# Optimization experiments

Hardware: AMD Instinct MI355X
Metric: run time of the kernel (lower is better)

The kernel has to match this reference:

```python
import jax, jax.numpy as jnp
import numpy as np

D_MODEL = 2048
N_HEADS = 16
HEAD_DIM = D_MODEL // N_HEADS  # 128
B, S, PAST = 2, 2048, 2048


def setup_inputs() -> dict:
    key = jax.random.key(0)
    ks = jax.random.split(key, 7)
    sc = 0.02
    return {
        "x": jax.random.normal(ks[0], (B, S, D_MODEL), dtype=jnp.float32),
        "past_k": jax.random.normal(ks[1], (B, N_HEADS, PAST, HEAD_DIM), dtype=jnp.float32),
        "past_v": jax.random.normal(ks[2], (B, N_HEADS, PAST, HEAD_DIM), dtype=jnp.float32),
        "Wq": jax.random.normal(ks[3], (D_MODEL, D_MODEL), dtype=jnp.float32) * sc,
        "Wk": jax.random.normal(ks[4], (D_MODEL, D_MODEL), dtype=jnp.float32) * sc,
        "Wv": jax.random.normal(ks[5], (D_MODEL, D_MODEL), dtype=jnp.float32) * sc,
        "Wo": jax.random.normal(ks[6], (D_MODEL, D_MODEL), dtype=jnp.float32) * sc,
    }


def reference(x, past_k, past_v, Wq, Wk, Wv, Wo):
    b, s, d = x.shape
    # nn.Linear(bias=False): y = x @ W.T ; split heads -> (B, H, S, hd)
    def proj_heads(W):
        return (x @ W.T).reshape(b, s, N_HEADS, HEAD_DIM).transpose(0, 2, 1, 3)
    q = proj_heads(Wq)
    k = proj_heads(Wk)
    v = proj_heads(Wv)
    # KV-cache append along sequence axis
    k = jnp.concatenate([past_k, k], axis=2)  # (B, H, full_S, hd)
    v = jnp.concatenate([past_v, v], axis=2)
    present = (k, v)
    full_s = k.shape[2]
    scores = jnp.einsum("bhqd,bhkd->bhqk", q, k) / (HEAD_DIM ** 0.5)
    # causal mask: query i (global pos past+i) may attend keys j <= past+i
    offset = full_s - s
    qi = jnp.arange(s)[:, None]
    kj = jnp.arange(full_s)[None, :]
    mask = kj > (qi + offset)  # triu with diagonal = full_s - s + 1
    scores = jnp.where(mask[None, None], -jnp.inf, scores)
    attn = jax.nn.softmax(scores, axis=-1)
    out = jnp.einsum("bhqk,bhkd->bhqd", attn, v)
    out = out.transpose(0, 2, 1, 3).reshape(b, s, d)
    output = out @ Wo.T
    return output, present
```

## Files before the change

### kernel.cpp

```cpp
#include <hip/hip_runtime.h>
#include <hip/hip_bf16.h>
#include <stdint.h>

typedef __attribute__((ext_vector_type(8))) short bf16x8;
typedef __attribute__((ext_vector_type(4))) float f32x4;
typedef __attribute__((ext_vector_type(16))) float f32x16;
typedef unsigned short u16;
typedef unsigned int u32;
typedef const __attribute__((address_space(1))) u32* gp_t;
typedef __attribute__((address_space(3))) u32* lp_t;

#define HD 128
#define NH 16
#define SEQ 2048
#define PASTN 2048
#define FULLS 4096
#define DM 2048

__device__ __forceinline__ u16 f2b(float f){
  union { float f; u32 u; } v; v.f = f;
  return (u16)((v.u + 0x7fffu + ((v.u >> 16) & 1u)) >> 16);
}
__device__ __forceinline__ float b2f(u16 b){
  union { u32 u; float f; } v; v.u = ((u32)b) << 16;
  return v.f;
}
__device__ __forceinline__ u32 cvtpk(float lo, float hi){
  u32 r; asm("v_cvt_pk_bf16_f32 %0, %1, %2" : "=v"(r) : "v"(lo), "v"(hi)); return r;
}
__device__ __forceinline__ f32x16 zero16(){ f32x16 z = {}; return z; }

__global__ void k_conv5(const float* __restrict__ sx,
                        const float* __restrict__ s1, const float* __restrict__ s2,
                        const float* __restrict__ s3, const float* __restrict__ s4,
                        u16* __restrict__ dx,
                        u16* __restrict__ d1, u16* __restrict__ d2,
                        u16* __restrict__ d3, u16* __restrict__ d4)
{
  const int total = 2097152 + 4 * 1048576;
  int i = blockIdx.x * blockDim.x + threadIdx.x;
  int stride = gridDim.x * blockDim.x;
  for (; i < total; i += stride){
    const float* s; u16* d; int off;
    if (i < 2097152){ s = sx; d = dx; off = i; }
    else {
      int t = i - 2097152;
      int seg = t >> 20; off = t & 1048575;
      s = (seg == 0) ? s1 : (seg == 1) ? s2 : (seg == 2) ? s3 : s4;
      d = (seg == 0) ? d1 : (seg == 1) ? d2 : (seg == 2) ? d3 : d4;
    }
    float4 v = ((const float4*)s)[off];
    ushort4 o = { f2b(v.x), f2b(v.y), f2b(v.z), f2b(v.w) };
    ((ushort4*)d)[off] = o;
  }
}

__global__ void k_past_k(const float* __restrict__ pk, float* __restrict__ outk,
                         u16* __restrict__ kb, int n4){
  int i = blockIdx.x * blockDim.x + threadIdx.x;
  int stride = gridDim.x * blockDim.x;
  for (; i < n4; i += stride){
    int g = i * 4;
    int c = g & 127;
    int r = g >> 7;
    int bh = r >> 11;
    int s = r & 2047;
    long dst = ((long)bh * FULLS + s) * HD + c;
    float4 v = ((const float4*)pk)[i];
    *(float4*)(outk + dst) = v;
    ushort4 o = { f2b(v.x), f2b(v.y), f2b(v.z), f2b(v.w) };
    *(ushort4*)(kb + dst) = o;
  }
}

__global__ void k_past_v(const float* __restrict__ pv, float* __restrict__ outv,
                         u16* __restrict__ vtb){
  __shared__ float tile[32][33];
  int bh = blockIdx.z;
  int d0 = blockIdx.x * 32;
  int s0 = blockIdx.y * 32;
  int tx = threadIdx.x, ty = threadIdx.y;
  const float* src = pv + (long)bh * PASTN * HD;
  float* dstv = outv + (long)bh * FULLS * HD;
#pragma unroll
  for (int k = 0; k < 4; k++){
    int si = ty + 8 * k;
    float v = src[(long)(s0 + si) * HD + d0 + tx];
    dstv[(long)(s0 + si) * HD + d0 + tx] = v;
    tile[si][tx] = v;
  }
  __syncthreads();
  u16* dstt = vtb + (long)bh * HD * FULLS;
#pragma unroll
  for (int k = 0; k < 4; k++){
    int di = ty + 8 * k;
    dstt[(long)(d0 + di) * FULLS + (s0 + tx)] = f2b(tile[tx][di]);
  }
}

__global__ void k_gemm_qkv(const u16* __restrict__ A,
                           const u16* __restrict__ Bq, const u16* __restrict__ Bk,
                           const u16* __restrict__ Bv,
                           u16* __restrict__ qb, u16* __restrict__ kbb,
                           u16* __restrict__ vtb,
                           float* __restrict__ outk, float* __restrict__ outv)
{
  __shared__ u16 As[128 * 64];
  __shared__ u16 Bs[128 * 64];
  const int K = DM;
  const int tid = threadIdx.x;
  const int w = tid >> 6, l = tid & 63;
  const int m0 = blockIdx.y * 128, n0 = blockIdx.x * 128;
  const int which = n0 >> 11;
  const u16* Bm = (which == 0) ? Bq : (which == 1) ? Bk : Bv;
  const int nbase = n0 & 2047;
  const int wr = w >> 1, wc = w & 1;
  const int lr = l & 15;
  const int lkb = (l >> 4) * 16;
  f32x4 acc[4][4] = {};

  for (int kt = 0; kt < K; kt += 64){
#pragma unroll
    for (int it = 0; it < 4; it++){
      int Pw = it * 4096 + w * 1024;
      int P = Pw + l * 16;
      int row = P >> 7, cb = P & 127;
      const u16* ga = A + (long)(m0 + row) * K + kt + (cb >> 1);
      __builtin_amdgcn_global_load_lds((gp_t)(const void*)ga, (lp_t)(void*)((char*)As + Pw), 16, 0, 0);
      const u16* gb = Bm + (long)(nbase + row) * K + kt + (cb >> 1);
      __builtin_amdgcn_global_load_lds((gp_t)(const void*)gb, (lp_t)(void*)((char*)Bs + Pw), 16, 0, 0);
    }
    __syncthreads();
#pragma unroll
    for (int kk = 0; kk < 2; kk++){
      bf16x8 af[4], bf[4];
#pragma unroll
      for (int i = 0; i < 4; i++){
        af[i] = *(const bf16x8*)((const char*)As + (wr * 64 + i * 16 + lr) * 128 + kk * 64 + lkb);
        bf[i] = *(const bf16x8*)((const char*)Bs + (wc * 64 + i * 16 + lr) * 128 + kk * 64 + lkb);
      }
#pragma unroll
      for (int i = 0; i < 4; i++)
#pragma unroll
        for (int j = 0; j < 4; j++)
          acc[i][j] = __builtin_amdgcn_mfma_f32_16x16x32_bf16(af[i], bf[j], acc[i][j], 0, 0, 0);
    }
    __syncthreads();
  }

  const int rbase = m0 + wr * 64 + ((l >> 4) << 2);
  const int cbase = wc * 64 + lr;
#pragma unroll
  for (int i = 0; i < 4; i++){
#pragma unroll
    for (int j = 0; j < 4; j++){
      const int nl = (nbase + cbase + j * 16);
      const int h = nl >> 7, dd = nl & 127;
      if (which == 2){
        const int mm = rbase + i * 16;
        const int b = mm >> 11, s = mm & 2047;
        const int bh = b * NH + h;
        ushort4 pk = { f2b(acc[i][j][0]), f2b(acc[i][j][1]), f2b(acc[i][j][2]), f2b(acc[i][j][3]) };
        *(ushort4*)(vtb + ((long)bh * HD + dd) * FULLS + PASTN + s) = pk;
#pragma unroll
        for (int r = 0; r < 4; r++){
          long idx = ((long)bh * FULLS + PASTN + s + r) * HD + dd;
          outv[idx] = acc[i][j][r];
        }
      } else if (which == 1){
#pragma unroll
        for (int r = 0; r < 4; r++){
          const int mm = rbase + i * 16 + r;
          const int b = mm >> 11, s = mm & 2047;
          long idx = (((long)(b * NH + h)) * FULLS + PASTN + s) * HD + dd;
          float v = acc[i][j][r];
          kbb[idx] = f2b(v);
          outk[idx] = v;
        }
      } else {
#pragma unroll
        for (int r = 0; r < 4; r++){
          const int mm = rbase + i * 16 + r;
          const int b = mm >> 11, s = mm & 2047;
          qb[(((long)(b * NH + h)) * SEQ + s) * HD + dd] = f2b(acc[i][j][r]);
        }
      }
    }
  }
}

__global__ void k_gemm_o(const u16* __restrict__ A, const u16* __restrict__ Bm,
                         float* __restrict__ outf, int M, int N, int K)
{
  __shared__ u16 As[128 * 64];
  __shared__ u16 Bs[128 * 64];
  const int tid = threadIdx.x;
  const int w = tid >> 6, l = tid & 63;
  const int m0 = blockIdx.y * 128, n0 = blockIdx.x * 128;
  const int wr = w >> 1, wc = w & 1;
  const int lr = l & 15;
  const int lkb = (l >> 4) * 16;
  f32x4 acc[4][4] = {};

  for (int kt = 0; kt < K; kt += 64){
#pragma unroll
    for (int it = 0; it < 4; it++){
      int Pw = it * 4096 + w * 1024;
      int P = Pw + l * 16;
      int row = P >> 7, cb = P & 127;
      const u16* ga = A + (long)(m0 + row) * K + kt + (cb >> 1);
      __builtin_amdgcn_global_load_lds((gp_t)(const void*)ga, (lp_t)(void*)((char*)As + Pw), 16, 0, 0);
      const u16* gb = Bm + (long)(n0 + row) * K + kt + (cb >> 1);
      __builtin_amdgcn_global_load_lds((gp_t)(const void*)gb, (lp_t)(void*)((char*)Bs + Pw), 16, 0, 0);
    }
    __syncthreads();
#pragma unroll
    for (int kk = 0; kk < 2; kk++){
      bf16x8 af[4], bf[4];
#pragma unroll
      for (int i = 0; i < 4; i++){
        af[i] = *(const bf16x8*)((const char*)As + (wr * 64 + i * 16 + lr) * 128 + kk * 64 + lkb);
        bf[i] = *(const bf16x8*)((const char*)Bs + (wc * 64 + i * 16 + lr) * 128 + kk * 64 + lkb);
      }
#pragma unroll
      for (int i = 0; i < 4; i++)
#pragma unroll
        for (int j = 0; j < 4; j++)
          acc[i][j] = __builtin_amdgcn_mfma_f32_16x16x32_bf16(af[i], bf[j], acc[i][j], 0, 0, 0);
    }
    __syncthreads();
  }

  const int rbase = m0 + wr * 64 + ((l >> 4) << 2);
  const int cbase = n0 + wc * 64 + lr;
#pragma unroll
  for (int i = 0; i < 4; i++)
#pragma unroll
    for (int j = 0; j < 4; j++){
      const int nn = cbase + j * 16;
#pragma unroll
      for (int r = 0; r < 4; r++)
        outf[(long)(rbase + i * 16 + r) * N + nn] = acc[i][j][r];
    }
}

__global__ __launch_bounds__(256, 2)
void k_attn(const u16* __restrict__ qb, const u16* __restrict__ kb,
            const u16* __restrict__ vtb, u16* __restrict__ ab)
{
  __shared__ u16 Ks[2][64 * 128];
  __shared__ u16 Vs[2][128 * 64];
  const int tid = threadIdx.x, w = tid >> 6, l = tid & 63;
  const int lq = l & 31, hi = l >> 5;
  const int dd0 = blockIdx.x;
  const int xcd = dd0 & 7;
  const int j   = dd0 >> 3;
  const int ja = j >> 5, jb = (j >> 1) & 15, jc = j & 1;
  const int bh  = xcd * 4 + 2 * ja + jc;
  const int q0b = ((ja ^ jc) ? (15 - jb) : jb) << 7;
  const int qbase = q0b + w * 32;
  const int qpos = PASTN + qbase + lq;
  const u16* qhead = qb + (long)bh * SEQ * HD;
  const u16* khead = kb + (long)bh * FULLS * HD;
  const u16* vhead = vtb + (long)bh * HD * FULLS;

  const float qscale = 0.08838834764831845f * 1.4426950408889634f;
  bf16x8 qf[8];
#pragma unroll
  for (int ks = 0; ks < 8; ks++){
    bf16x8 tq = *(const bf16x8*)(qhead + (long)(qbase + lq) * HD + ks * 16 + hi * 8);
#pragma unroll
    for (int jj = 0; jj < 8; jj++) tq[jj] = (short)f2b(b2f((u16)tq[jj]) * qscale);
    qf[ks] = tq;
  }

  const int kswz = (lq & 15) << 4;
  const int vswz = (lq & 7) << 4;
  const char* kaddr[8];
#pragma unroll
  for (int ks = 0; ks < 8; ks++)
    kaddr[ks] = (const char*)Ks + lq * 256 + ((ks * 32 + hi * 16) ^ kswz);
  const char* vaddr[4];
#pragma unroll
  for (int ks2 = 0; ks2 < 4; ks2++)
    vaddr[ks2] = (const char*)Vs + lq * 128 + ((ks2 * 32 + hi * 16) ^ vswz);

  int ksrcoff[4], vsrcoff[4];
#pragma unroll
  for (int it = 0; it < 4; it++){
    int P = it * 4096 + w * 1024 + l * 16;
    ksrcoff[it] = P ^ (((P >> 8) & 15) << 4);
    int row = P >> 7;
    int cb = (P & 127) ^ ((row & 7) << 4);
    vsrcoff[it] = row * 8192 + cb;
  }

  auto stageK = [&](int t, int bufo){
    const char* src = (const char*)khead + ((long)t << 14);
    char* dstb = (char*)Ks + bufo + w * 1024;
#pragma unroll
    for (int it = 0; it < 4; it++)
      __builtin_amdgcn_global_load_lds((gp_t)(const void*)(src + ksrcoff[it]),
                                       (lp_t)(void*)(dstb + it * 4096), 16, 0, 0);
  };
  auto stageV = [&](int t, int bufo){
    const char* src = (const char*)vhead + ((long)t << 7);
    char* dstb = (char*)Vs + bufo + w * 1024;
#pragma unroll
    for (int it = 0; it < 4; it++)
      __builtin_amdgcn_global_load_lds((gp_t)(const void*)(src + vsrcoff[it]),
                                       (lp_t)(void*)(dstb + it * 4096), 16, 0, 0);
  };

  f32x16 acc[4] = {};
  float m_run = -1e30f, l_run = 0.f;
  const int ntiles = (PASTN + q0b + 128) >> 6;

  auto finishPV = [&](f32x16& sp0, f32x16& sp1, int vbufo){
    float a0[8];
#pragma unroll
    for (int i = 0; i < 8; i++)
      a0[i] = fmaxf(fmaxf(sp0[i], sp0[i + 8]), fmaxf(sp1[i], sp1[i + 8]));
    float mx = fmaxf(fmaxf(fmaxf(a0[0], a0[1]), fmaxf(a0[2], a0[3])),
                     fmaxf(fmaxf(a0[4], a0[5]), fmaxf(a0[6], a0[7])));
    { float xa = mx, xb = mx;
      asm("v_permlane32_swap_b32 %0, %1" : "+v"(xa), "+v"(xb));
      mx = fmaxf(xa, xb); }

    if (!__all(mx <= m_run + 8.f)){
      float mnew = fmaxf(m_run, mx);
      float corr = __builtin_exp2f(m_run - mnew);
      m_run = mnew; l_run *= corr;
#pragma unroll
      for (int r = 0; r < 16; r++){
        int qlr = (r & 3) + 8 * (r >> 2) + 4 * hi;
        float cr = __shfl(corr, qlr);
#pragma unroll
        for (int d2 = 0; d2 < 4; d2++) acc[d2][r] *= cr;
      }
    }

    float rs = 0.f;
#pragma unroll
    for (int r = 0; r < 16; r++){
      sp0[r] = __builtin_exp2f(sp0[r] - m_run); rs += sp0[r];
      sp1[r] = __builtin_exp2f(sp1[r] - m_run); rs += sp1[r];
    }
    { float ra = rs, rb = rs;
      asm("v_permlane32_swap_b32 %0, %1" : "+v"(ra), "+v"(rb));
      l_run += ra + rb; }

    bf16x8 pfrag[4];
#pragma unroll
    for (int kb2 = 0; kb2 < 2; kb2++){
      const f32x16& sp = kb2 ? sp1 : sp0;
#pragma unroll
      for (int half = 0; half < 2; half++){
        const int h8 = half * 8;
        u32 A0 = cvtpk(sp[h8 + 0], sp[h8 + 1]);
        u32 A1 = cvtpk(sp[h8 + 2], sp[h8 + 3]);
        u32 B0 = cvtpk(sp[h8 + 4], sp[h8 + 5]);
        u32 B1 = cvtpk(sp[h8 + 6], sp[h8 + 7]);
        asm("v_permlane32_swap_b32 %0, %1" : "+v"(A0), "+v"(B0));
        asm("v_permlane32_swap_b32 %0, %1" : "+v"(A1), "+v"(B1));
        union { u32 wd[4]; bf16x8 v; } F;
        F.wd[0] = A0; F.wd[1] = A1; F.wd[2] = B0; F.wd[3] = B1;
        pfrag[kb2 * 2 + half] = F.v;
      }
    }

    __builtin_amdgcn_s_setprio(1);
#pragma unroll
    for (int ks2 = 0; ks2 < 4; ks2++)
#pragma unroll
      for (int d2 = 0; d2 < 4; d2++){
        bf16x8 vf = *(const bf16x8*)(vaddr[ks2] + vbufo + d2 * 4096);
        acc[d2] = __builtin_amdgcn_mfma_f32_32x32x16_bf16(pfrag[ks2], vf, acc[d2], 0, 0, 0);
      }
    __builtin_amdgcn_s_setprio(0);
  };

#define QKT_MASK(T_, BUFC_, SC0_, SC1_)                                        \
  {                                                                            \
    SC0_ = zero16(); SC1_ = zero16();                                          \
    __builtin_amdgcn_s_setprio(1);                                             \
    _Pragma("unroll")                                                          \
    for (int ks = 0; ks < 8; ks++){                                            \
      bf16x8 kf0 = *(const bf16x8*)(kaddr[ks] + (BUFC_));                      \
      bf16x8 kf1 = *(const bf16x8*)(kaddr[ks] + (BUFC_) + 8192);               \
      SC0_ = __builtin_amdgcn_mfma_f32_32x32x16_bf16(kf0, qf[ks], SC0_, 0,0,0);\
      SC1_ = __builtin_amdgcn_mfma_f32_32x32x16_bf16(kf1, qf[ks], SC1_, 0,0,0);\
    }                                                                          \
    __builtin_amdgcn_s_setprio(0);                                             \
    const int kvb_ = (T_) * 64;                                                \
    if (kvb_ + 63 > PASTN + qbase){                                            \
      _Pragma("unroll")                                                        \
      for (int r = 0; r < 16; r++){                                            \
        int key = kvb_ + (r & 3) + 8 * (r >> 2) + 4 * hi;                      \
        if (key > qpos) SC0_[r] = -1e30f;                                      \
        if (key + 32 > qpos) SC1_[r] = -1e30f;                                 \
      }                                                                        \
    }                                                                          \
  }

#define STEP(T_, BUFC_, SP0_, SP1_, SC0_, SC1_)                                \
  {                                                                            \
    if ((T_) + 1 < ntiles) stageK((T_) + 1, (BUFC_) ^ 16384);                  \
    QKT_MASK(T_, BUFC_, SC0_, SC1_);                                           \
    finishPV(SP0_, SP1_, (BUFC_) ^ 16384);                                     \
    __syncthreads();                                                           \
    if ((T_) + 1 < ntiles) stageV((T_) + 1, (BUFC_) ^ 16384);                  \
  }

  f32x16 PA0, PA1, PB0, PB1;

  stageK(0, 0); stageV(0, 0);
  __syncthreads();

  stageK(1, 16384);
  QKT_MASK(0, 0, PA0, PA1);
  __syncthreads();
  stageV(1, 16384);

  for (int t = 1; t + 2 < ntiles; t += 2){
    STEP(t,     16384, PA0, PA1, PB0, PB1);
    STEP(t + 1, 0,     PB0, PB1, PA0, PA1);
  }
  STEP(ntiles - 1, 16384, PA0, PA1, PB0, PB1);
  finishPV(PB0, PB1, 16384);

#undef STEP
#undef QKT_MASK

  float inv = 1.0f / l_run;
  const int b = bh >> 4, h = bh & 15;
#pragma unroll
  for (int r = 0; r < 16; r++){
    int qlr = (r & 3) + 8 * (r >> 2) + 4 * hi;
    float ir = __shfl(inv, qlr);
    long rowbase = ((long)b * SEQ + (qbase + qlr)) * DM + h * HD;
#pragma unroll
    for (int d2 = 0; d2 < 4; d2++)
      ab[rowbase + d2 * 32 + lq] = f2b(acc[d2][r] * ir);
  }
}

extern "C" void kernel_launch(void* const* d_in, const int* in_sizes, int n_in,
                              void* d_out, int out_size, void* d_ws, size_t ws_size,
                              hipStream_t stream) {
  const float* x      = (const float*)d_in[0];
  const float* past_k = (const float*)d_in[1];
  const float* past_v = (const float*)d_in[2];
  const float* Wq     = (const float*)d_in[3];
  const float* Wk     = (const float*)d_in[4];
  const float* Wv     = (const float*)d_in[5];
  const float* Wo     = (const float*)d_in[6];

  float* out  = (float*)d_out;
  float* outk = out + 8388608;
  float* outv = out + 25165824;

  char* ws = (char*)d_ws;
  u16* wqb = (u16*)ws;
  u16* wkb = (u16*)(ws + 8388608);
  u16* wvb = (u16*)(ws + 16777216);
  u16* wob = (u16*)(ws + 25165824);
  u16* xb  = (u16*)(ws + 33554432);
  u16* qb  = (u16*)(ws + 50331648);
  u16* kb  = (u16*)(ws + 67108864);
  u16* vtb = (u16*)(ws + 100663296);
  u16* ab  = xb;

  k_conv5<<<2048, 256, 0, stream>>>(x, Wq, Wk, Wv, Wo, xb, wqb, wkb, wvb, wob);
  k_past_k<<<2048, 256, 0, stream>>>(past_k, outk, kb, 2097152);
  k_past_v<<<dim3(4, 64, 32), dim3(32, 8), 0, stream>>>(past_v, outv, vtb);

  k_gemm_qkv<<<dim3(48, 32), 256, 0, stream>>>(xb, wqb, wkb, wvb,
                                               qb, kb, vtb, outk, outv);

  k_attn<<<512, 256, 0, stream>>>(qb, kb, vtb, ab);

  k_gemm_o<<<dim3(16, 32), 256, 0, stream>>>(ab, wob, out, 4096, 2048, 2048);
}
```

Measured before the change: 417.0 us.

## Rewrite QKV GEMM as 256x256-tile, 8-wave kernel with double-buffered swizzled LDS

Replaces the 128x128-tile QKV projection GEMM with a 512-thread kernel using 256x256 output tiles, a 128KB double-buffered LDS holding two K-chunks, and XOR-swizzled LDS layout to avoid bank conflicts. Global-to-LDS loads for the next K-chunk are interleaved with MFMA phases using fine-grained barriers, vmcnt waits and setprio. This aims to hide load latency and raise arithmetic intensity per block. The cost is one block per CU, fewer blocks (384), and higher register pressure from 32 accumulator fragments.

```diff
diff --git a/kernel.cpp b/kernel.cpp
--- a/kernel.cpp
+++ b/kernel.cpp
@@ -98,91 +98,153 @@
   }
 }
 
-__global__ void k_gemm_qkv(const u16* __restrict__ A,
-                           const u16* __restrict__ Bq, const u16* __restrict__ Bk,
-                           const u16* __restrict__ Bv,
-                           u16* __restrict__ qb, u16* __restrict__ kbb,
-                           u16* __restrict__ vtb,
-                           float* __restrict__ outk, float* __restrict__ outv)
+__global__ __launch_bounds__(512, 1)
+void k_gemm_qkv8(const u16* __restrict__ A,
+                 const u16* __restrict__ Bq, const u16* __restrict__ Bk,
+                 const u16* __restrict__ Bv,
+                 u16* __restrict__ qb, u16* __restrict__ kbb,
+                 u16* __restrict__ vtb,
+                 float* __restrict__ outk, float* __restrict__ outv)
 {
-  __shared__ u16 As[128 * 64];
-  __shared__ u16 Bs[128 * 64];
-  const int K = DM;
-  const int tid = threadIdx.x;
-  const int w = tid >> 6, l = tid & 63;
-  const int m0 = blockIdx.y * 128, n0 = blockIdx.x * 128;
-  const int which = n0 >> 11;
+  __shared__ char LDS[131072];
+  const int tid = threadIdx.x, w = tid >> 6, l = tid & 63;
+  const int wm = w >> 2, wn = w & 3;
+  const int m0 = blockIdx.y * 256;
+  const int which = blockIdx.x >> 3;
   const u16* Bm = (which == 0) ? Bq : (which == 1) ? Bk : Bv;
-  const int nbase = n0 & 2047;
-  const int wr = w >> 1, wc = w & 1;
-  const int lr = l & 15;
-  const int lkb = (l >> 4) * 16;
-  f32x4 acc[4][4] = {};
-
-  for (int kt = 0; kt < K; kt += 64){
-#pragma unroll
-    for (int it = 0; it < 4; it++){
-      int Pw = it * 4096 + w * 1024;
-      int P = Pw + l * 16;
-      int row = P >> 7, cb = P & 127;
-      const u16* ga = A + (long)(m0 + row) * K + kt + (cb >> 1);
-      __builtin_amdgcn_global_load_lds((gp_t)(const void*)ga, (lp_t)(void*)((char*)As + Pw), 16, 0, 0);
-      const u16* gb = Bm + (long)(nbase + row) * K + kt + (cb >> 1);
-      __builtin_amdgcn_global_load_lds((gp_t)(const void*)gb, (lp_t)(void*)((char*)Bs + Pw), 16, 0, 0);
-    }
-    __syncthreads();
-#pragma unroll
-    for (int kk = 0; kk < 2; kk++){
-      bf16x8 af[4], bf[4];
-#pragma unroll
-      for (int i = 0; i < 4; i++){
-        af[i] = *(const bf16x8*)((const char*)As + (wr * 64 + i * 16 + lr) * 128 + kk * 64 + lkb);
-        bf[i] = *(const bf16x8*)((const char*)Bs + (wc * 64 + i * 16 + lr) * 128 + kk * 64 + lkb);
-      }
-#pragma unroll
-      for (int i = 0; i < 4; i++)
-#pragma unroll
-        for (int j = 0; j < 4; j++)
-          acc[i][j] = __builtin_amdgcn_mfma_f32_16x16x32_bf16(af[i], bf[j], acc[i][j], 0, 0, 0);
-    }
-    __syncthreads();
-  }
-
-  const int rbase = m0 + wr * 64 + ((l >> 4) << 2);
-  const int cbase = wc * 64 + lr;
-#pragma unroll
-  for (int i = 0; i < 4; i++){
-#pragma unroll
-    for (int j = 0; j < 4; j++){
-      const int nl = (nbase + cbase + j * 16);
+  const int n0s = (blockIdx.x & 7) * 256;
+
+  const int aoff0 = (((l >> 4) * 16) ^ ((l & 7) << 4));
+  const int aoff1 = ((64 + (l >> 4) * 16) ^ ((l & 7) << 4));
+  const char* ArdB = LDS + wm * 16384 + (l & 15) * 128;
+  const char* BrdB = LDS + 65536 + (wn >> 1) * 16384 + (wn & 1) * 8192 + (l & 15) * 128;
+
+  const int Pa = tid * 16, Pb = tid * 16 + 8192;
+  const int ra = Pa >> 7, rb = Pb >> 7;
+  const int sro1 = ra * 2048 + ((((Pa & 127) ^ ((ra & 7) << 4))) >> 1);
+  const int sro2 = rb * 2048 + ((((Pb & 127) ^ ((rb & 7) << 4))) >> 1);
+  char* sd1 = LDS + w * 1024;
+  char* sd2 = LDS + w * 1024 + 8192;
+
+  f32x4 acc[8][4] = {};
+
+#define GLDS(SRC, DST) __builtin_amdgcn_global_load_lds((gp_t)(const void*)(SRC), (lp_t)(void*)(DST), 16, 0, 0)
+#define STG(MAT, ROWB, C, REG) { const u16* s_ = (MAT) + (long)(ROWB) * 2048 + (C) * 64; \
+    GLDS(s_ + sro1, sd1 + (REG)); GLDS(s_ + sro2, sd2 + (REG)); }
+#define RDB(DST, PAR) { _Pragma("unroll") for (int nf = 0; nf < 4; nf++){ \
+      DST[nf*2]   = *(const bf16x8*)(BrdB + (PAR)*32768 + nf*2048 + aoff0); \
+      DST[nf*2+1] = *(const bf16x8*)(BrdB + (PAR)*32768 + nf*2048 + aoff1); } }
+#define RDA(PAR, MF) \
+      a0 = *(const bf16x8*)(ArdB + (PAR)*32768 + (MF)*2048 + aoff0); \
+      a1 = *(const bf16x8*)(ArdB + (PAR)*32768 + (MF)*2048 + aoff1); \
+      a2 = *(const bf16x8*)(ArdB + (PAR)*32768 + (MF+1)*2048 + aoff0); \
+      a3 = *(const bf16x8*)(ArdB + (PAR)*32768 + (MF+1)*2048 + aoff1);
+#define BARW { __builtin_amdgcn_s_barrier(); \
+      asm volatile("s_waitcnt lgkmcnt(0)" ::: "memory"); \
+      __builtin_amdgcn_sched_barrier(0); }
+#define MM(BF, MF) { __builtin_amdgcn_s_setprio(1); \
+      _Pragma("unroll") for (int nf = 0; nf < 4; nf++){ \
+        acc[MF][nf]   = __builtin_amdgcn_mfma_f32_16x16x32_bf16(a0, BF[nf*2],   acc[MF][nf],   0,0,0); \
+        acc[MF][nf]   = __builtin_amdgcn_mfma_f32_16x16x32_bf16(a1, BF[nf*2+1], acc[MF][nf],   0,0,0); \
+        acc[MF+1][nf] = __builtin_amdgcn_mfma_f32_16x16x32_bf16(a2, BF[nf*2],   acc[MF+1][nf], 0,0,0); \
+        acc[MF+1][nf] = __builtin_amdgcn_mfma_f32_16x16x32_bf16(a3, BF[nf*2+1], acc[MF+1][nf], 0,0,0); } \
+      __builtin_amdgcn_s_setprio(0); }
+
+  STG(A,  m0,        0, 0);
+  STG(A,  m0 + 128,  0, 16384);
+  STG(Bm, n0s,       0, 65536);
+  STG(Bm, n0s + 128, 0, 81920);
+  STG(Bm, n0s,       1, 98304);
+  STG(Bm, n0s + 128, 1, 114688);
+  asm volatile("s_waitcnt vmcnt(4)" ::: "memory");
+  __builtin_amdgcn_s_barrier();
+
+  for (int i = 0; i < 16; ++i){
+    const int c1 = 2 * i + 1;
+    const int cn = 2 * i + 2;
+    const bool nlast = (i < 15);
+    bf16x8 b0[8], b1[8];
+    bf16x8 a0, a1, a2, a3;
+
+    RDB(b0, 0); RDA(0, 0);
+    STG(A, m0, c1, 32768);
+    BARW; MM(b0, 0);
+    __builtin_amdgcn_s_barrier();
+    RDA(0, 2);
+    STG(A, m0 + 128, c1, 49152);
+    BARW; MM(b0, 2);
+    __builtin_amdgcn_s_barrier();
+    RDA(0, 4);
+    if (nlast) STG(Bm, n0s, cn, 65536);
+    BARW; MM(b0, 4);
+    __builtin_amdgcn_s_barrier();
+    RDA(0, 6);
+    if (nlast) STG(Bm, n0s + 128, cn, 81920);
+    BARW; MM(b0, 6);
+    if (nlast) { asm volatile("s_waitcnt vmcnt(4)" ::: "memory"); }
+    else       { asm volatile("s_waitcnt vmcnt(0)" ::: "memory"); }
+    __builtin_amdgcn_s_barrier();
+    RDB(b1, 1); RDA(1, 0);
+    if (nlast) STG(A, m0, cn, 0);
+    BARW; MM(b1, 0);
+    __builtin_amdgcn_s_barrier();
+    RDA(1, 2);
+    if (nlast) STG(A, m0 + 128, cn, 16384);
+    BARW; MM(b1, 2);
+    __builtin_amdgcn_s_barrier();
+    RDA(1, 4);
+    if (nlast) STG(Bm, n0s, cn + 1, 98304);
+    BARW; MM(b1, 4);
+    __builtin_amdgcn_s_barrier();
+    RDA(1, 6);
+    if (nlast) STG(Bm, n0s + 128, cn + 1, 114688);
+    BARW; MM(b1, 6);
+    if (nlast) { asm volatile("s_waitcnt vmcnt(4)" ::: "memory"); }
+    __builtin_amdgcn_s_barrier();
+  }
+
+#undef MM
+#undef BARW
+#undef RDA
+#undef RDB
+#undef STG
+#undef GLDS
+
+  const int rbase = m0 + wm * 128 + ((l >> 4) << 2);
+  const int cb2 = n0s + wn * 64 + (l & 15);
+#pragma unroll
+  for (int mf = 0; mf < 8; mf++){
+#pragma unroll
+    for (int nf = 0; nf < 4; nf++){
+      const int nl = cb2 + nf * 16;
       const int h = nl >> 7, dd = nl & 127;
       if (which == 2){
-        const int mm = rbase + i * 16;
+        const int mm = rbase + mf * 16;
         const int b = mm >> 11, s = mm & 2047;
         const int bh = b * NH + h;
-        ushort4 pk = { f2b(acc[i][j][0]), f2b(acc[i][j][1]), f2b(acc[i][j][2]), f2b(acc[i][j][3]) };
+        ushort4 pk = { f2b(acc[mf][nf][0]), f2b(acc[mf][nf][1]), f2b(acc[mf][nf][2]), f2b(acc[mf][nf][3]) };
         *(ushort4*)(vtb + ((long)bh * HD + dd) * FULLS + PASTN + s) = pk;
 #pragma unroll
         for (int r = 0; r < 4; r++){
           long idx = ((long)bh * FULLS + PASTN + s + r) * HD + dd;
-          outv[idx] = acc[i][j][r];
+          outv[idx] = acc[mf][nf][r];
         }
       } else if (which == 1){
 #pragma unroll
         for (int r = 0; r < 4; r++){
-          const int mm = rbase + i * 16 + r;
+          const int mm = rbase + mf * 16 + r;
           const int b = mm >> 11, s = mm & 2047;
           long idx = (((long)(b * NH + h)) * FULLS + PASTN + s) * HD + dd;
-          float v = acc[i][j][r];
+          float v = acc[mf][nf][r];
           kbb[idx] = f2b(v);
           outk[idx] = v;
         }
       } else {
 #pragma unroll
         for (int r = 0; r < 4; r++){
-          const int mm = rbase + i * 16 + r;
+          const int mm = rbase + mf * 16 + r;
           const int b = mm >> 11, s = mm & 2047;
-          qb[(((long)(b * NH + h)) * SEQ + s) * HD + dd] = f2b(acc[i][j][r]);
+          qb[(((long)(b * NH + h)) * SEQ + s) * HD + dd] = f2b(acc[mf][nf][r]);
         }
       }
     }
@@ -475,8 +537,8 @@
   k_past_k<<<2048, 256, 0, stream>>>(past_k, outk, kb, 2097152);
   k_past_v<<<dim3(4, 64, 32), dim3(32, 8), 0, stream>>>(past_v, outv, vtb);
 
-  k_gemm_qkv<<<dim3(48, 32), 256, 0, stream>>>(xb, wqb, wkb, wvb,
-                                               qb, kb, vtb, outk, outv);
+  k_gemm_qkv8<<<dim3(24, 16), 512, 0, stream>>>(xb, wqb, wkb, wvb,
+                                                qb, kb, vtb, outk, outv);
 
   k_attn<<<512, 256, 0, stream>>>(qb, kb, vtb, ab);
 
```

Measured after the change: 402.1 us. -3.6%, faster.
